# Kernel optimization log

Measured on AMD Instinct MI355X. Metric: run time of the kernel, lower is better.

Reference implementation:

```python
import jax, jax.numpy as jnp
import numpy as np

B, T, D, H = 4, 2048, 1024, 16
HD = D // H
EPS = 1e-5
NEG = 1e10


def setup_inputs() -> dict:
    key = jax.random.key(0)
    k1, k2, k3 = jax.random.split(key, 3)
    return {
        "target": jax.random.normal(k1, (B, T, D), dtype=jnp.float32),
        "w_qkv": jax.random.normal(k2, (D, 3 * D), dtype=jnp.float32) * 0.02,
        "w_proj": jax.random.normal(k3, (D, D), dtype=jnp.float32) * (0.02 / np.sqrt(24.0)),
        "b_proj": jnp.zeros((D,), dtype=jnp.float32),
        "ln_gamma": jnp.ones((D,), dtype=jnp.float32),
        "ln_beta": jnp.zeros((D,), dtype=jnp.float32),
    }


def reference(target, w_qkv, w_proj, b_proj, ln_gamma, ln_beta):
    b, t, d = target.shape
    resid = target
    qkv = target @ w_qkv                      # [B,T,3D]
    q, k, v = jnp.split(qkv, 3, axis=-1)
    # [B,H,T,hd]
    q = q.reshape(b, t, H, HD).transpose(0, 2, 1, 3)
    k = k.reshape(b, t, H, HD).transpose(0, 2, 1, 3)
    v = v.reshape(b, t, H, HD).transpose(0, 2, 1, 3)
    scores = jnp.einsum("bhqd,bhkd->bhqk", q, k) * (1.0 / np.sqrt(HD))
    causal = (jnp.arange(t)[:, None] >= jnp.arange(t)[None, :]).astype(scores.dtype)
    scores = scores * causal - (1.0 - causal) * NEG
    attn = jax.nn.softmax(scores, axis=-1)
    out = jnp.einsum("bhqk,bhkd->bhqd", attn, v)
    out = out.transpose(0, 2, 1, 3).reshape(b, t, d)
    proj = out @ w_proj + b_proj
    x = proj + resid
    mu = jnp.mean(x, axis=-1, keepdims=True)
    var = jnp.var(x, axis=-1, keepdims=True)
    return ((x - mu) * jax.lax.rsqrt(var + EPS)) * ln_gamma + ln_beta
```

## Files before the change

### kernel.cpp

```cpp
#include <hip/hip_runtime.h>
#include <hip/hip_bf16.h>

#define Bsz 4
#define Tseq 2048
#define Dmodel 1024
#define Hn 16
#define HD 64
#define EPS 1e-5f
#define QSCALE 0.18033688011112042f

typedef __attribute__((ext_vector_type(8))) short bf16x8;
typedef __attribute__((ext_vector_type(4))) short bf16x4;
typedef __attribute__((ext_vector_type(4))) float f32x4;
typedef __attribute__((ext_vector_type(4))) unsigned short us4;
typedef __attribute__((ext_vector_type(2))) unsigned uint2v;

typedef const __attribute__((address_space(1))) void* gas_t;
typedef __attribute__((address_space(3))) void* las_t;

__device__ __forceinline__ unsigned short f2bf(float x) {
    unsigned u = __builtin_bit_cast(unsigned, x);
    u += 0x7fffu + ((u >> 16) & 1u);
    return (unsigned short)(u >> 16);
}
__device__ __forceinline__ unsigned pack2bf_t(float a, float b) {
    return (__builtin_bit_cast(unsigned, a) >> 16)
         | (__builtin_bit_cast(unsigned, b) & 0xffff0000u);
}

__device__ __forceinline__ f32x4 mfma16x16x16(bf16x4 a, bf16x4 b, f32x4 c) {
#if __has_builtin(__builtin_amdgcn_mfma_f32_16x16x16bf16_1k)
    return __builtin_amdgcn_mfma_f32_16x16x16bf16_1k(a, b, c, 0, 0, 0);
#else
    asm("v_mfma_f32_16x16x16_bf16 %0, %1, %2, %0" : "+v"(c) : "v"(a), "v"(b));
    return c;
#endif
}

__global__ void cast_bf16(const float* __restrict__ in, unsigned short* __restrict__ out) {
    int i = (blockIdx.x * 256 + threadIdx.x) * 4;
    float4 v = *(const float4*)(in + i);
    us4 o = { f2bf(v.x), f2bf(v.y), f2bf(v.z), f2bf(v.w) };
    *(us4*)(out + i) = o;
}

__global__ void transpose_cast(const float* __restrict__ in, unsigned short* __restrict__ out,
                               int K, int N) {
    __shared__ unsigned short t[32][33];
    int k0 = blockIdx.y * 32, n0 = blockIdx.x * 32;
    int tx = threadIdx.x, ty = threadIdx.y;
    #pragma unroll
    for (int i = 0; i < 32; i += 8)
        t[ty + i][tx] = f2bf(in[(size_t)(k0 + ty + i) * N + n0 + tx]);
    __syncthreads();
    #pragma unroll
    for (int i = 0; i < 32; i += 8)
        out[(size_t)(n0 + ty + i) * K + k0 + tx] = t[tx][ty + i];
}

template<bool OUT_BF16, bool SCALEQ>
__global__ __launch_bounds__(256)
void gemm_mfma(const unsigned short* __restrict__ A,
               const unsigned short* __restrict__ Bt,
               void* __restrict__ Cv, int M, int N, int K,
               const float* __restrict__ bias, const float* __restrict__ resid) {
    __shared__ unsigned short As[128 * 32];
    __shared__ unsigned short Bs[128 * 32];
    const int tid = threadIdx.x;
    const int w = tid >> 6, lane = tid & 63;
    const int l16 = lane & 15, quad = lane >> 4;

    const int lin = blockIdx.y * gridDim.x + blockIdx.x;
    const int chunk = (gridDim.x * gridDim.y) >> 3;
    const int neff = (lin & 7) * chunk + (lin >> 3);
    const int bx = neff % gridDim.x, by = neff / gridDim.x;
    const int m0 = by * 128, n0 = bx * 128;

    f32x4 acc[4][4];
    #pragma unroll
    for (int i = 0; i < 4; ++i)
        #pragma unroll
        for (int j = 0; j < 4; ++j)
            acc[i][j] = f32x4{0.f, 0.f, 0.f, 0.f};

    const int lrow = lane >> 2, lcol = lane & 3;
    const unsigned short* ag = A  + (size_t)(m0 + w * 32 + lrow) * K + lcol * 8;
    const unsigned short* bg = Bt + (size_t)(n0 + w * 32 + lrow) * K + lcol * 8;
    unsigned short* al0 = As + (w * 32) * 32;
    unsigned short* al1 = As + (w * 32 + 16) * 32;
    unsigned short* bl0 = Bs + (w * 32) * 32;
    unsigned short* bl1 = Bs + (w * 32 + 16) * 32;
    const int am = (w >> 1) * 64, bn = (w & 1) * 64;

    for (int k0 = 0; k0 < K; k0 += 32) {
        __builtin_amdgcn_global_load_lds((gas_t)(ag + k0),          (las_t)al0, 16, 0, 0);
        __builtin_amdgcn_global_load_lds((gas_t)(ag + 16 * K + k0), (las_t)al1, 16, 0, 0);
        __builtin_amdgcn_global_load_lds((gas_t)(bg + k0),          (las_t)bl0, 16, 0, 0);
        __builtin_amdgcn_global_load_lds((gas_t)(bg + 16 * K + k0), (las_t)bl1, 16, 0, 0);
        __syncthreads();

        bf16x8 af[4], bf[4];
        #pragma unroll
        for (int i = 0; i < 4; ++i)
            af[i] = *(const bf16x8*)&As[(am + i * 16 + l16) * 32 + quad * 8];
        #pragma unroll
        for (int j = 0; j < 4; ++j)
            bf[j] = *(const bf16x8*)&Bs[(bn + j * 16 + l16) * 32 + quad * 8];
        #pragma unroll
        for (int i = 0; i < 4; ++i)
            #pragma unroll
            for (int j = 0; j < 4; ++j)
                acc[i][j] = __builtin_amdgcn_mfma_f32_16x16x32_bf16(af[i], bf[j], acc[i][j], 0, 0, 0);
        __syncthreads();
    }

    #pragma unroll
    for (int i = 0; i < 4; ++i) {
        #pragma unroll
        for (int j = 0; j < 4; ++j) {
            const int col = n0 + bn + j * 16 + l16;
            const float scale = (SCALEQ && col < Dmodel) ? QSCALE : 1.0f;
            #pragma unroll
            for (int r = 0; r < 4; ++r) {
                const int row = m0 + am + i * 16 + quad * 4 + r;
                if (OUT_BF16) {
                    ((unsigned short*)Cv)[(size_t)row * N + col] = f2bf(acc[i][j][r] * scale);
                } else {
                    float v = acc[i][j][r] + bias[col] + resid[(size_t)row * N + col];
                    ((float*)Cv)[(size_t)row * N + col] = v;
                }
            }
        }
    }
}

__global__ __launch_bounds__(256)
void flash_attn(const unsigned short* __restrict__ qkv, unsigned short* __restrict__ out) {
    const int lin = blockIdx.y * gridDim.x + blockIdx.x;
    const int xcd = lin & 7, local = lin >> 3;
    const int bh = xcd + 8 * (local & 7);
    const int x = local >> 3;
    const int qt_lo = x, qt_hi = (Tseq / 64 - 1) - x;
    const int h = bh & (Hn - 1), b = bh >> 4;
    const int tid = threadIdx.x;
    const int wave = tid >> 6;
    const int lane = tid & 63;
    const int l16 = lane & 15;
    const int quad = lane >> 4;

    __shared__ unsigned short Ks[2][2][64 * 32];
    __shared__ unsigned short Vs[2][64 * 64];

    const unsigned short* qrow = qkv + ((size_t)(b * Tseq + wave * 16 + l16)) * 3072 + h * HD;
    const unsigned short* qhi = qrow + (size_t)qt_hi * 64 * 3072;
    const unsigned short* qlo = qrow + (size_t)qt_lo * 64 * 3072;
    bf16x8 qh0 = *(const bf16x8*)(qhi + quad * 8);
    bf16x8 qh1 = *(const bf16x8*)(qhi + 32 + quad * 8);
    bf16x8 ql0 = *(const bf16x8*)(qlo + quad * 8);
    bf16x8 ql1 = *(const bf16x8*)(qlo + 32 + quad * 8);

    float l_hi = 0.f, l_lo = 0.f;
    f32x4 ohi[4], olo[4];
    #pragma unroll
    for (int nt = 0; nt < 4; ++nt) {
        ohi[nt] = f32x4{0.f, 0.f, 0.f, 0.f};
        olo[nt] = f32x4{0.f, 0.f, 0.f, 0.f};
    }

    const unsigned short* kbase = qkv + (size_t)b * Tseq * 3072 + Dmodel + h * HD;
    const unsigned short* vbase = kbase + Dmodel;
    const unsigned short* kg = kbase + (size_t)(wave * 16 + (lane >> 2)) * 3072 + (lane & 3) * 8;
    const int vp = tid >> 3, vc = tid & 7;
    const unsigned short* vsrc = vbase + (size_t)(2 * vp) * 3072 + vc * 8;

    auto stageK = [&](int buf, size_t koff) {
        __builtin_amdgcn_global_load_lds((gas_t)(kg + koff),
                                         (las_t)&Ks[buf][0][wave * 16 * 32], 16, 0, 0);
        __builtin_amdgcn_global_load_lds((gas_t)(kg + koff + 32),
                                         (las_t)&Ks[buf][1][wave * 16 * 32], 16, 0, 0);
    };
    auto writeV = [&](int buf, const bf16x8& va, const bf16x8& vb) {
        const int kc = vp >> 2;
        const int kin = (2 * vp) & 7;
        #pragma unroll
        for (int j = 0; j < 8; ++j) {
            const int d = vc * 8 + j;
            const int pc = kc ^ ((d + (d >> 3)) & 7);
            unsigned pk = (unsigned)(unsigned short)va[j]
                        | ((unsigned)(unsigned short)vb[j] << 16);
            *(unsigned*)&Vs[buf][d * 64 + pc * 8 + kin] = pk;
        }
    };

    auto compute = [&](int buf, int q0t, const bf16x8& qf0, const bf16x8& qf1,
                       f32x4* oacc, float& l_part, bool diag, int k0g) {
        __builtin_amdgcn_s_setprio(1);
        f32x4 st[4];
        #pragma unroll
        for (int nt = 0; nt < 4; ++nt) {
            f32x4 a = {0.f, 0.f, 0.f, 0.f};
            bf16x8 kf0 = *(const bf16x8*)&Ks[buf][0][(nt * 16 + l16) * 32 + quad * 8];
            a = __builtin_amdgcn_mfma_f32_16x16x32_bf16(kf0, qf0, a, 0, 0, 0);
            bf16x8 kf1 = *(const bf16x8*)&Ks[buf][1][(nt * 16 + l16) * 32 + quad * 8];
            a = __builtin_amdgcn_mfma_f32_16x16x32_bf16(kf1, qf1, a, 0, 0, 0);
            st[nt] = a;
        }
        if (diag) {
            const int qg = q0t + wave * 16 + l16;
            #pragma unroll
            for (int nt = 0; nt < 4; ++nt) {
                const int kgl = k0g + nt * 16 + quad * 4;
                #pragma unroll
                for (int r = 0; r < 4; ++r)
                    if (kgl + r > qg) st[nt][r] = -1e30f;
            }
        }
        bf16x4 pa[4];
        #pragma unroll
        for (int nt = 0; nt < 4; ++nt) {
            float p0 = exp2f(st[nt][0]);
            float p1 = exp2f(st[nt][1]);
            float p2 = exp2f(st[nt][2]);
            float p3 = exp2f(st[nt][3]);
            l_part += (p0 + p1) + (p2 + p3);
            uint2v t;
            t.x = pack2bf_t(p0, p1);
            t.y = pack2bf_t(p2, p3);
            pa[nt] = __builtin_bit_cast(bf16x4, t);
        }
        #pragma unroll
        for (int ntk = 0; ntk < 4; ++ntk) {
            const int k0 = ntk * 16 + quad * 4;
            const int chunk = k0 >> 3;
            const int kin = k0 & 7;
            #pragma unroll
            for (int ntd = 0; ntd < 4; ++ntd) {
                const int d = ntd * 16 + l16;
                const int pc = chunk ^ ((d + (d >> 3)) & 7);
                bf16x4 vf = *(const bf16x4*)&Vs[buf][d * 64 + pc * 8 + kin];
                oacc[ntd] = mfma16x16x16(pa[ntk], vf, oacc[ntd]);
            }
        }
        __builtin_amdgcn_s_setprio(0);
    };

    stageK(0, 0);
    bf16x8 va = *(const bf16x8*)(vsrc);
    bf16x8 vb = *(const bf16x8*)(vsrc + 3072);
    writeV(0, va, vb);
    __syncthreads();

    int cur = 0;
    for (int kt = 0; kt <= qt_hi; ++kt) {
        if (kt < qt_hi) {
            const size_t koff_n = (size_t)(kt + 1) * 64 * 3072;
            stageK(cur ^ 1, koff_n);
            va = *(const bf16x8*)(vsrc + koff_n);
            vb = *(const bf16x8*)(vsrc + koff_n + 3072);
        }

        compute(cur, qt_hi * 64, qh0, qh1, ohi, l_hi, kt == qt_hi, kt * 64);
        if (kt <= qt_lo)
            compute(cur, qt_lo * 64, ql0, ql1, olo, l_lo, kt == qt_lo, kt * 64);

        if (kt < qt_hi) writeV(cur ^ 1, va, vb);
        __syncthreads();
        cur ^= 1;
    }

    auto epilogue = [&](int q0t, f32x4* oacc, float l_part) {
        l_part += __shfl_xor(l_part, 16, 64);
        l_part += __shfl_xor(l_part, 32, 64);
        float inv[4];
        #pragma unroll
        for (int r = 0; r < 4; ++r) {
            float lr = __shfl(l_part, quad * 4 + r, 64);
            inv[r] = __builtin_amdgcn_rcpf(lr);
        }
        unsigned short* obase =
            out + ((size_t)(b * Tseq + q0t + wave * 16)) * Dmodel + h * HD;
        #pragma unroll
        for (int nt = 0; nt < 4; ++nt) {
            #pragma unroll
            for (int r = 0; r < 4; ++r) {
                int row = quad * 4 + r;
                obase[(size_t)row * Dmodel + nt * 16 + l16] = f2bf(oacc[nt][r] * inv[r]);
            }
        }
    };
    epilogue(qt_hi * 64, ohi, l_hi);
    epilogue(qt_lo * 64, olo, l_lo);
}

__global__ void ln_kernel(float* __restrict__ x, const float* __restrict__ gamma,
                          const float* __restrict__ beta) {
    const int row = blockIdx.x;
    float* xr = x + (size_t)row * Dmodel;
    const int tid = threadIdx.x;
    __shared__ float rs[256], rs2[256];

    float4 v = *(const float4*)(xr + tid * 4);
    float s  = v.x + v.y + v.z + v.w;
    float s2 = v.x * v.x + v.y * v.y + v.z * v.z + v.w * v.w;
    rs[tid] = s; rs2[tid] = s2;
    __syncthreads();
    for (int off = 128; off; off >>= 1) {
        if (tid < off) { rs[tid] += rs[tid + off]; rs2[tid] += rs2[tid + off]; }
        __syncthreads();
    }
    const float mu  = rs[0] * (1.0f / Dmodel);
    const float var = rs2[0] * (1.0f / Dmodel) - mu * mu;
    const float rstd = rsqrtf(var + EPS);

    float4 g = *(const float4*)(gamma + tid * 4);
    float4 bt = *(const float4*)(beta + tid * 4);
    float4 o;
    o.x = (v.x - mu) * rstd * g.x + bt.x;
    o.y = (v.y - mu) * rstd * g.y + bt.y;
    o.z = (v.z - mu) * rstd * g.z + bt.z;
    o.w = (v.w - mu) * rstd * g.w + bt.w;
    *(float4*)(xr + tid * 4) = o;
}

extern "C" void kernel_launch(void* const* d_in, const int* in_sizes, int n_in,
                              void* d_out, int out_size, void* d_ws, size_t ws_size,
                              hipStream_t stream) {
    const float* target   = (const float*)d_in[0];
    const float* w_qkv    = (const float*)d_in[1];
    const float* w_proj   = (const float*)d_in[2];
    const float* b_proj   = (const float*)d_in[3];
    const float* ln_gamma = (const float*)d_in[4];
    const float* ln_beta  = (const float*)d_in[5];
    float* out = (float*)d_out;

    const int M = Bsz * Tseq;

    char* ws = (char*)d_ws;
    unsigned short* qkv_bf16 = (unsigned short*)(ws);
    unsigned short* attn_bf  = (unsigned short*)(ws + 48ull * 1024 * 1024);
    unsigned short* tgt_bf   = (unsigned short*)(ws + 64ull * 1024 * 1024);
    unsigned short* wqT      = (unsigned short*)(ws + 80ull * 1024 * 1024);
    unsigned short* wpT      = (unsigned short*)(ws + 86ull * 1024 * 1024);

    cast_bf16<<<dim3(M * Dmodel / 1024), 256, 0, stream>>>(target, tgt_bf);
    transpose_cast<<<dim3(3072 / 32, Dmodel / 32), dim3(32, 8), 0, stream>>>(
        w_qkv, wqT, Dmodel, 3072);
    transpose_cast<<<dim3(Dmodel / 32, Dmodel / 32), dim3(32, 8), 0, stream>>>(
        w_proj, wpT, Dmodel, Dmodel);

    gemm_mfma<true, true><<<dim3(3072 / 128, M / 128), 256, 0, stream>>>(
        tgt_bf, wqT, qkv_bf16, M, 3072, Dmodel, nullptr, nullptr);

    flash_attn<<<dim3(Tseq / 128, Bsz * Hn), 256, 0, stream>>>(qkv_bf16, attn_bf);

    gemm_mfma<false, false><<<dim3(Dmodel / 128, M / 128), 256, 0, stream>>>(
        attn_bf, wpT, out, M, Dmodel, Dmodel, b_proj, target);

    ln_kernel<<<dim3(M), 256, 0, stream>>>(out, ln_gamma, ln_beta);
}
```

Before: 295.7 us.

## Deepen GEMM K-step, use raw exp2, perm packing and precomputed V offsets

The GEMM now loads a 64-wide K slab per iteration into two LDS halves, which halves the number of barrier pairs per K loop. The attention softmax uses the raw hardware exp2 instruction instead of exp2f and packs bf16 pairs with a single byte-permute. The swizzled V LDS addresses are precomputed once per thread as byte offsets and XORed per k-tile. The extra LDS in the GEMM may reduce occupancy, and raw exp2 skips the denormal/range handling that exp2f provides.

```diff
diff --git a/kernel.cpp b/kernel.cpp
--- a/kernel.cpp
+++ b/kernel.cpp
@@ -24,8 +24,18 @@
     return (unsigned short)(u >> 16);
 }
 __device__ __forceinline__ unsigned pack2bf_t(float a, float b) {
-    return (__builtin_bit_cast(unsigned, a) >> 16)
-         | (__builtin_bit_cast(unsigned, b) & 0xffff0000u);
+    return __builtin_amdgcn_perm(__builtin_bit_cast(unsigned, b),
+                                 __builtin_bit_cast(unsigned, a), 0x07060302u);
+}
+
+__device__ __forceinline__ float exp2_raw(float x) {
+#if __has_builtin(__builtin_amdgcn_exp2f)
+    return __builtin_amdgcn_exp2f(x);
+#else
+    float r;
+    asm("v_exp_f32 %0, %1" : "=v"(r) : "v"(x));
+    return r;
+#endif
 }
 
 __device__ __forceinline__ f32x4 mfma16x16x16(bf16x4 a, bf16x4 b, f32x4 c) {
@@ -64,8 +74,8 @@
                const unsigned short* __restrict__ Bt,
                void* __restrict__ Cv, int M, int N, int K,
                const float* __restrict__ bias, const float* __restrict__ resid) {
-    __shared__ unsigned short As[128 * 32];
-    __shared__ unsigned short Bs[128 * 32];
+    __shared__ unsigned short As[2][128 * 32];
+    __shared__ unsigned short Bs[2][128 * 32];
     const int tid = threadIdx.x;
     const int w = tid >> 6, lane = tid & 63;
     const int l16 = lane & 15, quad = lane >> 4;
@@ -86,31 +96,42 @@
     const int lrow = lane >> 2, lcol = lane & 3;
     const unsigned short* ag = A  + (size_t)(m0 + w * 32 + lrow) * K + lcol * 8;
     const unsigned short* bg = Bt + (size_t)(n0 + w * 32 + lrow) * K + lcol * 8;
-    unsigned short* al0 = As + (w * 32) * 32;
-    unsigned short* al1 = As + (w * 32 + 16) * 32;
-    unsigned short* bl0 = Bs + (w * 32) * 32;
-    unsigned short* bl1 = Bs + (w * 32 + 16) * 32;
+    unsigned short* al0 = As[0] + (w * 32) * 32;
+    unsigned short* al1 = As[0] + (w * 32 + 16) * 32;
+    unsigned short* ah0 = As[1] + (w * 32) * 32;
+    unsigned short* ah1 = As[1] + (w * 32 + 16) * 32;
+    unsigned short* bl0 = Bs[0] + (w * 32) * 32;
+    unsigned short* bl1 = Bs[0] + (w * 32 + 16) * 32;
+    unsigned short* bh0 = Bs[1] + (w * 32) * 32;
+    unsigned short* bh1 = Bs[1] + (w * 32 + 16) * 32;
     const int am = (w >> 1) * 64, bn = (w & 1) * 64;
 
-    for (int k0 = 0; k0 < K; k0 += 32) {
-        __builtin_amdgcn_global_load_lds((gas_t)(ag + k0),          (las_t)al0, 16, 0, 0);
-        __builtin_amdgcn_global_load_lds((gas_t)(ag + 16 * K + k0), (las_t)al1, 16, 0, 0);
-        __builtin_amdgcn_global_load_lds((gas_t)(bg + k0),          (las_t)bl0, 16, 0, 0);
-        __builtin_amdgcn_global_load_lds((gas_t)(bg + 16 * K + k0), (las_t)bl1, 16, 0, 0);
+    for (int k0 = 0; k0 < K; k0 += 64) {
+        __builtin_amdgcn_global_load_lds((gas_t)(ag + k0),               (las_t)al0, 16, 0, 0);
+        __builtin_amdgcn_global_load_lds((gas_t)(ag + 16 * K + k0),      (las_t)al1, 16, 0, 0);
+        __builtin_amdgcn_global_load_lds((gas_t)(ag + k0 + 32),          (las_t)ah0, 16, 0, 0);
+        __builtin_amdgcn_global_load_lds((gas_t)(ag + 16 * K + k0 + 32), (las_t)ah1, 16, 0, 0);
+        __builtin_amdgcn_global_load_lds((gas_t)(bg + k0),               (las_t)bl0, 16, 0, 0);
+        __builtin_amdgcn_global_load_lds((gas_t)(bg + 16 * K + k0),      (las_t)bl1, 16, 0, 0);
+        __builtin_amdgcn_global_load_lds((gas_t)(bg + k0 + 32),          (las_t)bh0, 16, 0, 0);
+        __builtin_amdgcn_global_load_lds((gas_t)(bg + 16 * K + k0 + 32), (las_t)bh1, 16, 0, 0);
         __syncthreads();
 
-        bf16x8 af[4], bf[4];
-        #pragma unroll
-        for (int i = 0; i < 4; ++i)
-            af[i] = *(const bf16x8*)&As[(am + i * 16 + l16) * 32 + quad * 8];
-        #pragma unroll
-        for (int j = 0; j < 4; ++j)
-            bf[j] = *(const bf16x8*)&Bs[(bn + j * 16 + l16) * 32 + quad * 8];
-        #pragma unroll
-        for (int i = 0; i < 4; ++i)
+        #pragma unroll
+        for (int ks = 0; ks < 2; ++ks) {
+            bf16x8 af[4], bf[4];
+            #pragma unroll
+            for (int i = 0; i < 4; ++i)
+                af[i] = *(const bf16x8*)&As[ks][(am + i * 16 + l16) * 32 + quad * 8];
             #pragma unroll
             for (int j = 0; j < 4; ++j)
-                acc[i][j] = __builtin_amdgcn_mfma_f32_16x16x32_bf16(af[i], bf[j], acc[i][j], 0, 0, 0);
+                bf[j] = *(const bf16x8*)&Bs[ks][(bn + j * 16 + l16) * 32 + quad * 8];
+            #pragma unroll
+            for (int i = 0; i < 4; ++i)
+                #pragma unroll
+                for (int j = 0; j < 4; ++j)
+                    acc[i][j] = __builtin_amdgcn_mfma_f32_16x16x32_bf16(af[i], bf[j], acc[i][j], 0, 0, 0);
+        }
         __syncthreads();
     }
 
@@ -167,6 +188,15 @@
         olo[nt] = f32x4{0.f, 0.f, 0.f, 0.f};
     }
 
+    unsigned vrb[4];
+    #pragma unroll
+    for (int ntd = 0; ntd < 4; ++ntd) {
+        const int d = ntd * 16 + l16;
+        const int X = (d + (d >> 3)) & 7;
+        vrb[ntd] = (unsigned)(d * 128 + (quad & 1) * 8)
+                 ^ (unsigned)(X << 4) ^ (unsigned)((quad >> 1) << 4);
+    }
+
     const unsigned short* kbase = qkv + (size_t)b * Tseq * 3072 + Dmodel + h * HD;
     const unsigned short* vbase = kbase + Dmodel;
     const unsigned short* kg = kbase + (size_t)(wave * 16 + (lane >> 2)) * 3072 + (lane & 3) * 8;
@@ -218,26 +248,22 @@
         bf16x4 pa[4];
         #pragma unroll
         for (int nt = 0; nt < 4; ++nt) {
-            float p0 = exp2f(st[nt][0]);
-            float p1 = exp2f(st[nt][1]);
-            float p2 = exp2f(st[nt][2]);
-            float p3 = exp2f(st[nt][3]);
+            float p0 = exp2_raw(st[nt][0]);
+            float p1 = exp2_raw(st[nt][1]);
+            float p2 = exp2_raw(st[nt][2]);
+            float p3 = exp2_raw(st[nt][3]);
             l_part += (p0 + p1) + (p2 + p3);
             uint2v t;
             t.x = pack2bf_t(p0, p1);
             t.y = pack2bf_t(p2, p3);
             pa[nt] = __builtin_bit_cast(bf16x4, t);
         }
+        const char* vsb = (const char*)&Vs[buf][0];
         #pragma unroll
         for (int ntk = 0; ntk < 4; ++ntk) {
-            const int k0 = ntk * 16 + quad * 4;
-            const int chunk = k0 >> 3;
-            const int kin = k0 & 7;
             #pragma unroll
             for (int ntd = 0; ntd < 4; ++ntd) {
-                const int d = ntd * 16 + l16;
-                const int pc = chunk ^ ((d + (d >> 3)) & 7);
-                bf16x4 vf = *(const bf16x4*)&Vs[buf][d * 64 + pc * 8 + kin];
+                bf16x4 vf = *(const bf16x4*)(vsb + (vrb[ntd] ^ (unsigned)(ntk << 5)));
                 oacc[ntd] = mfma16x16x16(pa[ntk], vf, oacc[ntd]);
             }
         }
@@ -351,7 +377,7 @@
     gemm_mfma<true, true><<<dim3(3072 / 128, M / 128), 256, 0, stream>>>(
         tgt_bf, wqT, qkv_bf16, M, 3072, Dmodel, nullptr, nullptr);
 
-    flash_attn<<<dim3(Tseq / 128, Bsz * Hn), 256, 0, stream>>>(qkv_bf16, attn_bf);
+    flash_attn<<<dim3(16, Bsz * Hn), 256, 0, stream>>>(qkv_bf16, attn_bf);
 
     gemm_mfma<false, false><<<dim3(Dmodel / 128, M / 128), 256, 0, stream>>>(
         attn_bf, wpT, out, M, Dmodel, Dmodel, b_proj, target);
```

Result: faster. 272.3 us (-7.9%).
